# Kernel optimization log

Hardware: AMD Instinct MI355X
Metric: run time of the kernel (lower is better)

The kernel has to match this reference:

```python
import jax, jax.numpy as jnp
import numpy as np

TOP_K = 2


def setup_inputs() -> dict:
    key = jax.random.key(0)
    k_x, k_g, k_w1, k_w2, k_w3 = jax.random.split(key, 5)
    B, S, D, H, E = 2, 512, 1024, 512, 8
    x = jax.random.normal(k_x, (B, S, D), dtype=jnp.float32)
    gate_w = jax.random.normal(k_g, (D, E), dtype=jnp.float32) * (D ** -0.5)
    w1 = jax.random.normal(k_w1, (E, D, H), dtype=jnp.float32) * 0.02  # gate proj
    w2 = jax.random.normal(k_w2, (E, H, D), dtype=jnp.float32) * 0.02  # down proj
    w3 = jax.random.normal(k_w3, (E, D, H), dtype=jnp.float32) * 0.02  # up proj
    return {"x": x, "gate_w": gate_w, "w1": w1, "w2": w2, "w3": w3}


def reference(x, gate_w, w1, w2, w3):
    # Token-choice top-k MoE with grouped SwiGLU experts, no shared expert.
    # Equivalent to torchtune MoE: gather routed tokens, scale by top-k router
    # score, run per-expert FFN, scatter-add back. Since each expert's FFN has
    # no bias (FFN(0) == 0), the dispatch/grouped-GEMM/combine is expressed
    # densely as sum_e FFN_e(scale[:, e] * x), which is mathematically identical.
    B, S, D = x.shape
    E = gate_w.shape[1]
    xf = x.reshape(B * S, D)                      # [T, D]
    T = B * S

    logits = xf @ gate_w                          # [T, E]
    scores = jax.nn.softmax(logits, axis=-1)
    top_scores, top_idx = jax.lax.top_k(scores, TOP_K)  # [T, k]

    # scale[t, e] = router score if expert e selected for token t, else 0
    scale = jnp.zeros((T, E), dtype=x.dtype).at[
        jnp.arange(T)[:, None], top_idx
    ].set(top_scores)

    xs = scale.T[:, :, None] * xf[None, :, :]     # [E, T, D] scaled routed input
    h = jax.nn.silu(jnp.einsum('etd,edh->eth', xs, w1)) \
        * jnp.einsum('etd,edh->eth', xs, w3)      # [E, T, H]
    y = jnp.einsum('eth,ehd->etd', h, w2)         # [E, T, D]
    out = y.sum(axis=0)                           # combine (scatter-add equiv)
    return out.reshape(B, S, D)
```

## Files before the change

### kernel.cpp

```cpp
#include <hip/hip_runtime.h>
#include <hip/hip_bf16.h>
#include <cstddef>

#define T_TOK 1024
#define D_DIM 1024
#define H_DIM 512
#define E_EXP 8
#define P_CAP 2560
#define MAX_MT 72
#define LDA 72

typedef __attribute__((ext_vector_type(4))) float    float4_t;
typedef __attribute__((ext_vector_type(8))) short    short8_t;
typedef __attribute__((ext_vector_type(4))) unsigned uint4_t;

__device__ __forceinline__ short f2bf(float f) {
  union { float f; unsigned u; } v; v.f = f;
  unsigned u = v.u;
  u += 0x7FFFu + ((u >> 16) & 1u);
  return (short)(u >> 16);
}

__device__ __forceinline__ unsigned pkbf(float a, float b) {
  union { __hip_bfloat162 h; unsigned u; } v;
  v.h = __float22bfloat162_rn(make_float2(a, b));
  return v.u;
}

__global__ __launch_bounds__(256) void prep_kernel(
    const float* __restrict__ w1, const float* __restrict__ w3,
    const float* __restrict__ w2, const float* __restrict__ x,
    const float* __restrict__ gw, short* __restrict__ w13t,
    short* __restrict__ w2t, int* __restrict__ idx2,
    float* __restrict__ scale2, float* __restrict__ out) {
  __shared__ float tile[64][69];
  const int z = blockIdx.z;
  const int tid = threadIdx.x;

  if (z < 24) {
    const float* src; short* dst; int N, ldd, row_off;
    if (z < 16) {
      if (blockIdx.y >= 8) return;
      int which = z >> 3, e = z & 7;
      src = (which ? w3 : w1) + (size_t)e * D_DIM * H_DIM;
      dst = w13t + (size_t)e * D_DIM * (2 * H_DIM);
      N = H_DIM; ldd = D_DIM; row_off = which ? H_DIM : 0;
    } else {
      if (blockIdx.x >= 8) return;
      int e = z - 16;
      src = w2 + (size_t)e * H_DIM * D_DIM;
      dst = w2t + (size_t)e * D_DIM * H_DIM;
      N = D_DIM; ldd = H_DIM; row_off = 0;
    }
    const int k0 = blockIdx.x * 64, n0 = blockIdx.y * 64;
    const int kr = tid >> 4, nc = (tid & 15) * 4;
    #pragma unroll
    for (int p = 0; p < 4; ++p) {
      int k = p * 16 + kr;
      float4_t v = *(const float4_t*)(src + (size_t)(k0 + k) * N + n0 + nc);
      tile[k][nc]     = v[0];
      tile[k][nc + 1] = v[1];
      tile[k][nc + 2] = v[2];
      tile[k][nc + 3] = v[3];
    }
    __syncthreads();
    const int r8 = tid >> 3, c8 = tid & 7;
    #pragma unroll
    for (int p = 0; p < 2; ++p) {
      int row = p * 32 + r8;
      uint4_t u;
      #pragma unroll
      for (int jj = 0; jj < 4; ++jj)
        u[jj] = pkbf(tile[c8 * 8 + 2 * jj][row], tile[c8 * 8 + 2 * jj + 1][row]);
      *(uint4_t*)(dst + (size_t)(row_off + n0 + row) * ldd + k0 + c8 * 8) = u;
    }
    return;
  }

  if (z == 25) {
    float4_t z4 = {0.f, 0.f, 0.f, 0.f};
    float4_t* o = (float4_t*)(out + ((size_t)(blockIdx.y * 16 + blockIdx.x)) * 4096);
    #pragma unroll
    for (int i = 0; i < 4; ++i) o[i * 256 + tid] = z4;
    return;
  }

  const int wid  = tid >> 6;
  const int lane = tid & 63;
  const int t = (blockIdx.y * 16 + blockIdx.x) * 4 + wid;
  const float* xr = x + (size_t)t * D_DIM;
  float acc[E_EXP];
  #pragma unroll
  for (int e = 0; e < E_EXP; ++e) acc[e] = 0.f;
  for (int d = lane; d < D_DIM; d += 64) {
    float xv = xr[d];
    float4_t g0 = *(const float4_t*)(gw + d * E_EXP);
    float4_t g1 = *(const float4_t*)(gw + d * E_EXP + 4);
    acc[0] += xv * g0[0]; acc[1] += xv * g0[1];
    acc[2] += xv * g0[2]; acc[3] += xv * g0[3];
    acc[4] += xv * g1[0]; acc[5] += xv * g1[1];
    acc[6] += xv * g1[2]; acc[7] += xv * g1[3];
  }
  #pragma unroll
  for (int off = 32; off >= 1; off >>= 1) {
    #pragma unroll
    for (int e = 0; e < E_EXP; ++e) acc[e] += __shfl_down(acc[e], off, 64);
  }
  if (lane == 0) {
    float m = acc[0];
    #pragma unroll
    for (int e = 1; e < E_EXP; ++e) m = fmaxf(m, acc[e]);
    float p[E_EXP]; float s = 0.f;
    #pragma unroll
    for (int e = 0; e < E_EXP; ++e) { p[e] = __expf(acc[e] - m); s += p[e]; }
    float inv = 1.f / s;
    #pragma unroll
    for (int e = 0; e < E_EXP; ++e) p[e] *= inv;
    int i1 = 0;
    #pragma unroll
    for (int e = 1; e < E_EXP; ++e) if (p[e] > p[i1]) i1 = e;
    int i2 = (i1 == 0) ? 1 : 0;
    #pragma unroll
    for (int e = 0; e < E_EXP; ++e) {
      if (e == i1 || e == i2) continue;
      if (p[e] > p[i2]) i2 = e;
    }
    idx2[2 * t]     = i1;  scale2[2 * t]     = p[i1];
    idx2[2 * t + 1] = i2;  scale2[2 * t + 1] = p[i2];
  }
}

__global__ __launch_bounds__(256) void scan_kernel(
    const int* __restrict__ idx2, const float* __restrict__ scale2,
    int* __restrict__ pair_tok, float* __restrict__ pair_scale,
    int* __restrict__ meta) {
  __shared__ int cnt[E_EXP], base[E_EXP], cur[E_EXP];
  const int tid = threadIdx.x;
  if (tid < E_EXP) { cnt[tid] = 0; cur[tid] = 0; }
  for (int p = tid; p < P_CAP; p += 256) { pair_tok[p] = -1; pair_scale[p] = 0.f; }
  __syncthreads();
  for (int t = tid; t < T_TOK; t += 256) {
    atomicAdd(&cnt[idx2[2 * t]], 1);
    atomicAdd(&cnt[idx2[2 * t + 1]], 1);
  }
  __syncthreads();
  if (tid == 0) {
    int b = 0, g = 0;
    for (int e = 0; e < E_EXP; ++e) {
      base[e] = b;
      int al = (cnt[e] + 31) & ~31;
      for (int j = 0; j < al; j += 32) { meta[1 + g] = e; meta[81 + g] = b + j; ++g; }
      b += al;
    }
    meta[0] = g;
  }
  __syncthreads();
  for (int t = tid; t < T_TOK; t += 256) {
    #pragma unroll
    for (int s = 0; s < 2; ++s) {
      int e = idx2[2 * t + s];
      int p = base[e] + atomicAdd(&cur[e], 1);
      pair_tok[p] = t;
      pair_scale[p] = scale2[2 * t + s];
    }
  }
}

__global__ __launch_bounds__(256, 6) void gemm1_kernel(
    const float* __restrict__ x, const short* __restrict__ w13t,
    const int* __restrict__ pair_tok, const float* __restrict__ pair_scale,
    const int* __restrict__ meta, short* __restrict__ h) {
  __shared__ short As[32 * LDA];
  __shared__ short B1s[32 * LDA];
  __shared__ short B3s[32 * LDA];
  const int mt = blockIdx.y;
  if (mt >= meta[0]) return;
  const int e    = meta[1 + mt];
  const int row0 = meta[81 + mt];
  const int n0   = blockIdx.x * 32;
  const int tid = threadIdx.x, lane = tid & 63, wid = tid >> 6;
  const int wr = wid >> 1, wc = wid & 1;
  const int q = lane >> 4, ln = lane & 15;
  const short* bsrc = w13t + (size_t)e * D_DIM * (2 * H_DIM);

  const int ar = tid >> 3, ak = (tid & 7) * 8;
  const int   tokr = pair_tok[row0 + ar];
  const float sc   = pair_scale[row0 + ar];
  const float* xrow = x + (size_t)(tokr < 0 ? 0 : tokr) * D_DIM + ak;
  const int br = tid >> 3, bu = (tid & 7) * 8;
  const short* b1p = bsrc + (size_t)(n0 + br) * D_DIM + bu;
  const short* b3p = bsrc + (size_t)(H_DIM + n0 + br) * D_DIM + bu;

  float4_t acc1 = {0.f, 0.f, 0.f, 0.f}, acc3 = {0.f, 0.f, 0.f, 0.f};

  for (int k0 = 0; k0 < D_DIM; k0 += 64) {
    float4_t v0 = *(const float4_t*)(xrow + k0);
    float4_t v1 = *(const float4_t*)(xrow + k0 + 4);
    uint4_t vb1 = *(const uint4_t*)(b1p + k0);
    uint4_t vb3 = *(const uint4_t*)(b3p + k0);
    uint4_t u0 = {pkbf(v0[0] * sc, v0[1] * sc), pkbf(v0[2] * sc, v0[3] * sc),
                  pkbf(v1[0] * sc, v1[1] * sc), pkbf(v1[2] * sc, v1[3] * sc)};
    *(uint4_t*)&As[ar * LDA + ak]  = u0;
    *(uint4_t*)&B1s[br * LDA + bu] = vb1;
    *(uint4_t*)&B3s[br * LDA + bu] = vb3;
    __syncthreads();

    short8_t af[2], b1f[2], b3f[2];
    #pragma unroll
    for (int kk = 0; kk < 2; ++kk) {
      af[kk]  = *(const short8_t*)&As[(wr * 16 + ln) * LDA + kk * 32 + q * 8];
      b1f[kk] = *(const short8_t*)&B1s[(wc * 16 + ln) * LDA + kk * 32 + q * 8];
      b3f[kk] = *(const short8_t*)&B3s[(wc * 16 + ln) * LDA + kk * 32 + q * 8];
    }
    #pragma unroll
    for (int kk = 0; kk < 2; ++kk) {
      acc1 = __builtin_amdgcn_mfma_f32_16x16x32_bf16(af[kk], b1f[kk], acc1, 0, 0, 0);
      acc3 = __builtin_amdgcn_mfma_f32_16x16x32_bf16(af[kk], b3f[kk], acc3, 0, 0, 0);
    }
    __syncthreads();
  }

  {
    int r_base = row0 + wr * 16 + q * 4;
    int col = n0 + wc * 16 + ln;
    #pragma unroll
    for (int rr = 0; rr < 4; ++rr) {
      float c1 = acc1[rr];
      float c3 = acc3[rr];
      float sig = 1.f / (1.f + __expf(-c1));
      h[(size_t)(r_base + rr) * H_DIM + col] = f2bf(c1 * sig * c3);
    }
  }
}

__global__ __launch_bounds__(256, 6) void gemm2_kernel(
    const short* __restrict__ h, const short* __restrict__ w2t,
    const int* __restrict__ pair_tok, const int* __restrict__ meta,
    float* __restrict__ out) {
  __shared__ short As[32 * LDA];
  __shared__ short Bs[64 * LDA];
  const int mt = blockIdx.y;
  if (mt >= meta[0]) return;
  const int e    = meta[1 + mt];
  const int row0 = meta[81 + mt];
  const int n0   = blockIdx.x * 64;
  const int tid = threadIdx.x, lane = tid & 63, wid = tid >> 6;
  const int wr = wid >> 1, wc = wid & 1;
  const int q = lane >> 4, ln = lane & 15;
  const short* bsrc = w2t + (size_t)e * D_DIM * H_DIM;

  const int ar = tid >> 3, ak = (tid & 7) * 8;
  const short* arow = h + (size_t)(row0 + ar) * H_DIM + ak;
  const int br = tid >> 2, bk = (tid & 3) * 16;
  const short* brow = bsrc + (size_t)(n0 + br) * H_DIM + bk;

  float4_t acc[2];
  acc[0] = acc[1] = (float4_t){0.f, 0.f, 0.f, 0.f};

  for (int k0 = 0; k0 < H_DIM; k0 += 64) {
    uint4_t va  = *(const uint4_t*)(arow + k0);
    uint4_t vb0 = *(const uint4_t*)(brow + k0);
    uint4_t vb1 = *(const uint4_t*)(brow + k0 + 8);
    *(uint4_t*)&As[ar * LDA + ak]     = va;
    *(uint4_t*)&Bs[br * LDA + bk]     = vb0;
    *(uint4_t*)&Bs[br * LDA + bk + 8] = vb1;
    __syncthreads();

    short8_t af[2], bf[2][2];
    #pragma unroll
    for (int kk = 0; kk < 2; ++kk) {
      af[kk] = *(const short8_t*)&As[(wr * 16 + ln) * LDA + kk * 32 + q * 8];
      #pragma unroll
      for (int j = 0; j < 2; ++j)
        bf[j][kk] = *(const short8_t*)&Bs[(wc * 32 + j * 16 + ln) * LDA + kk * 32 + q * 8];
    }
    #pragma unroll
    for (int j = 0; j < 2; ++j)
      #pragma unroll
      for (int kk = 0; kk < 2; ++kk)
        acc[j] = __builtin_amdgcn_mfma_f32_16x16x32_bf16(af[kk], bf[j][kk], acc[j], 0, 0, 0);
    __syncthreads();
  }

  {
    int r_base = row0 + wr * 16 + q * 4;
    #pragma unroll
    for (int rr = 0; rr < 4; ++rr) {
      int tok = pair_tok[r_base + rr];
      if (tok < 0) continue;
      float* orow = out + (size_t)tok * D_DIM;
      #pragma unroll
      for (int j = 0; j < 2; ++j) {
        int col = n0 + wc * 32 + j * 16 + ln;
        atomicAdd(orow + col, acc[j][rr]);
      }
    }
  }
}

extern "C" void kernel_launch(void* const* d_in, const int* in_sizes, int n_in,
                              void* d_out, int out_size, void* d_ws, size_t ws_size,
                              hipStream_t stream) {
  const float* x  = (const float*)d_in[0];
  const float* gw = (const float*)d_in[1];
  const float* w1 = (const float*)d_in[2];
  const float* w2 = (const float*)d_in[3];
  const float* w3 = (const float*)d_in[4];
  float* out = (float*)d_out;

  char* ws = (char*)d_ws;
  int*   idx2    = (int*)  (ws);
  float* scale2  = (float*)(ws + 8192);
  int*   ptok    = (int*)  (ws + 16384);
  float* pscale  = (float*)(ws + 32768);
  int*   meta    = (int*)  (ws + 49152);
  short* h       = (short*)(ws + (1u << 20));
  short* w13t    = (short*)(ws + (4u << 20));
  short* w2t     = (short*)(ws + (21u << 20));

  prep_kernel<<<dim3(16, 16, 26), dim3(256), 0, stream>>>(
      w1, w3, w2, x, gw, w13t, w2t, idx2, scale2, out);
  scan_kernel<<<dim3(1), dim3(256), 0, stream>>>(idx2, scale2, ptok, pscale, meta);
  gemm1_kernel<<<dim3(H_DIM / 32, MAX_MT), dim3(256), 0, stream>>>(
      x, w13t, ptok, pscale, meta, h);
  gemm2_kernel<<<dim3(D_DIM / 64, MAX_MT), dim3(256), 0, stream>>>(
      h, w2t, ptok, meta, out);
}
```

Before: 146.7 us.

## Double-buffer LDS in both GEMMs and pre-stage scaled bf16 routed activations

```diff
diff --git a/kernel.cpp b/kernel.cpp
--- a/kernel.cpp
+++ b/kernel.cpp
@@ -9,10 +9,13 @@
 #define P_CAP 2560
 #define MAX_MT 72
 #define LDA 72
+#define NK1 16
+#define NK2 8
 
 typedef __attribute__((ext_vector_type(4))) float    float4_t;
 typedef __attribute__((ext_vector_type(8))) short    short8_t;
 typedef __attribute__((ext_vector_type(4))) unsigned uint4_t;
+typedef __attribute__((ext_vector_type(2))) unsigned uint2_t;
 
 __device__ __forceinline__ short f2bf(float f) {
   union { float f; unsigned u; } v; v.f = f;
@@ -166,13 +169,31 @@
   }
 }
 
-__global__ __launch_bounds__(256, 6) void gemm1_kernel(
-    const float* __restrict__ x, const short* __restrict__ w13t,
-    const int* __restrict__ pair_tok, const float* __restrict__ pair_scale,
+__global__ __launch_bounds__(256) void astage_kernel(
+    const float* __restrict__ x, const int* __restrict__ pair_tok,
+    const float* __restrict__ pair_scale, short* __restrict__ Ag) {
+  const int tid = threadIdx.x;
+  const int row = blockIdx.x * 8 + (tid >> 5);
+  const int c0  = (tid & 31) * 4;
+  const int   tok = pair_tok[row];
+  const float sc  = pair_scale[row];
+  const float* xr = x + (size_t)(tok < 0 ? 0 : tok) * D_DIM;
+  short* orow = Ag + (size_t)row * D_DIM;
+  #pragma unroll
+  for (int j = 0; j < 8; ++j) {
+    int c = c0 + j * 128;
+    float4_t v = *(const float4_t*)(xr + c);
+    uint2_t u = { pkbf(v[0] * sc, v[1] * sc), pkbf(v[2] * sc, v[3] * sc) };
+    *(uint2_t*)(orow + c) = u;
+  }
+}
+
+__global__ __launch_bounds__(256, 5) void gemm1_kernel(
+    const short* __restrict__ Ag, const short* __restrict__ w13t,
     const int* __restrict__ meta, short* __restrict__ h) {
-  __shared__ short As[32 * LDA];
-  __shared__ short B1s[32 * LDA];
-  __shared__ short B3s[32 * LDA];
+  __shared__ short As[2][32 * LDA];
+  __shared__ short B1s[2][32 * LDA];
+  __shared__ short B3s[2][32 * LDA];
   const int mt = blockIdx.y;
   if (mt >= meta[0]) return;
   const int e    = meta[1 + mt];
@@ -183,41 +204,60 @@
   const int q = lane >> 4, ln = lane & 15;
   const short* bsrc = w13t + (size_t)e * D_DIM * (2 * H_DIM);
 
-  const int ar = tid >> 3, ak = (tid & 7) * 8;
-  const int   tokr = pair_tok[row0 + ar];
-  const float sc   = pair_scale[row0 + ar];
-  const float* xrow = x + (size_t)(tokr < 0 ? 0 : tokr) * D_DIM + ak;
-  const int br = tid >> 3, bu = (tid & 7) * 8;
-  const short* b1p = bsrc + (size_t)(n0 + br) * D_DIM + bu;
-  const short* b3p = bsrc + (size_t)(H_DIM + n0 + br) * D_DIM + bu;
+  const int sr = tid >> 3, sk = (tid & 7) * 8;
+  const short* ap  = Ag   + (size_t)(row0 + sr) * D_DIM + sk;
+  const short* b1p = bsrc + (size_t)(n0 + sr) * D_DIM + sk;
+  const short* b3p = bsrc + (size_t)(H_DIM + n0 + sr) * D_DIM + sk;
 
   float4_t acc1 = {0.f, 0.f, 0.f, 0.f}, acc3 = {0.f, 0.f, 0.f, 0.f};
 
-  for (int k0 = 0; k0 < D_DIM; k0 += 64) {
-    float4_t v0 = *(const float4_t*)(xrow + k0);
-    float4_t v1 = *(const float4_t*)(xrow + k0 + 4);
-    uint4_t vb1 = *(const uint4_t*)(b1p + k0);
-    uint4_t vb3 = *(const uint4_t*)(b3p + k0);
-    uint4_t u0 = {pkbf(v0[0] * sc, v0[1] * sc), pkbf(v0[2] * sc, v0[3] * sc),
-                  pkbf(v1[0] * sc, v1[1] * sc), pkbf(v1[2] * sc, v1[3] * sc)};
-    *(uint4_t*)&As[ar * LDA + ak]  = u0;
-    *(uint4_t*)&B1s[br * LDA + bu] = vb1;
-    *(uint4_t*)&B3s[br * LDA + bu] = vb3;
+  {
+    uint4_t va = *(const uint4_t*)ap;
+    uint4_t v1 = *(const uint4_t*)b1p;
+    uint4_t v3 = *(const uint4_t*)b3p;
+    *(uint4_t*)&As[0][sr * LDA + sk]  = va;
+    *(uint4_t*)&B1s[0][sr * LDA + sk] = v1;
+    *(uint4_t*)&B3s[0][sr * LDA + sk] = v3;
+  }
+
+  for (int t = 0; t < NK1 - 1; ++t) {
     __syncthreads();
+    const int cur = t & 1, nxt = cur ^ 1;
+    const int ko = (t + 1) * 64;
+    uint4_t wa  = *(const uint4_t*)(ap + ko);
+    uint4_t w1v = *(const uint4_t*)(b1p + ko);
+    uint4_t w3v = *(const uint4_t*)(b3p + ko);
 
     short8_t af[2], b1f[2], b3f[2];
     #pragma unroll
     for (int kk = 0; kk < 2; ++kk) {
-      af[kk]  = *(const short8_t*)&As[(wr * 16 + ln) * LDA + kk * 32 + q * 8];
-      b1f[kk] = *(const short8_t*)&B1s[(wc * 16 + ln) * LDA + kk * 32 + q * 8];
-      b3f[kk] = *(const short8_t*)&B3s[(wc * 16 + ln) * LDA + kk * 32 + q * 8];
+      af[kk]  = *(const short8_t*)&As[cur][(wr * 16 + ln) * LDA + kk * 32 + q * 8];
+      b1f[kk] = *(const short8_t*)&B1s[cur][(wc * 16 + ln) * LDA + kk * 32 + q * 8];
+      b3f[kk] = *(const short8_t*)&B3s[cur][(wc * 16 + ln) * LDA + kk * 32 + q * 8];
     }
     #pragma unroll
     for (int kk = 0; kk < 2; ++kk) {
       acc1 = __builtin_amdgcn_mfma_f32_16x16x32_bf16(af[kk], b1f[kk], acc1, 0, 0, 0);
       acc3 = __builtin_amdgcn_mfma_f32_16x16x32_bf16(af[kk], b3f[kk], acc3, 0, 0, 0);
     }
-    __syncthreads();
+    *(uint4_t*)&As[nxt][sr * LDA + sk]  = wa;
+    *(uint4_t*)&B1s[nxt][sr * LDA + sk] = w1v;
+    *(uint4_t*)&B3s[nxt][sr * LDA + sk] = w3v;
+  }
+  __syncthreads();
+  {
+    short8_t af[2], b1f[2], b3f[2];
+    #pragma unroll
+    for (int kk = 0; kk < 2; ++kk) {
+      af[kk]  = *(const short8_t*)&As[1][(wr * 16 + ln) * LDA + kk * 32 + q * 8];
+      b1f[kk] = *(const short8_t*)&B1s[1][(wc * 16 + ln) * LDA + kk * 32 + q * 8];
+      b3f[kk] = *(const short8_t*)&B3s[1][(wc * 16 + ln) * LDA + kk * 32 + q * 8];
+    }
+    #pragma unroll
+    for (int kk = 0; kk < 2; ++kk) {
+      acc1 = __builtin_amdgcn_mfma_f32_16x16x32_bf16(af[kk], b1f[kk], acc1, 0, 0, 0);
+      acc3 = __builtin_amdgcn_mfma_f32_16x16x32_bf16(af[kk], b3f[kk], acc3, 0, 0, 0);
+    }
   }
 
   {
@@ -233,12 +273,12 @@
   }
 }
 
-__global__ __launch_bounds__(256, 6) void gemm2_kernel(
+__global__ __launch_bounds__(256, 5) void gemm2_kernel(
     const short* __restrict__ h, const short* __restrict__ w2t,
     const int* __restrict__ pair_tok, const int* __restrict__ meta,
     float* __restrict__ out) {
-  __shared__ short As[32 * LDA];
-  __shared__ short Bs[64 * LDA];
+  __shared__ short As[2][32 * LDA];
+  __shared__ short Bs[2][64 * LDA];
   const int mt = blockIdx.y;
   if (mt >= meta[0]) return;
   const int e    = meta[1 + mt];
@@ -257,29 +297,56 @@
   float4_t acc[2];
   acc[0] = acc[1] = (float4_t){0.f, 0.f, 0.f, 0.f};
 
-  for (int k0 = 0; k0 < H_DIM; k0 += 64) {
-    uint4_t va  = *(const uint4_t*)(arow + k0);
-    uint4_t vb0 = *(const uint4_t*)(brow + k0);
-    uint4_t vb1 = *(const uint4_t*)(brow + k0 + 8);
-    *(uint4_t*)&As[ar * LDA + ak]     = va;
-    *(uint4_t*)&Bs[br * LDA + bk]     = vb0;
-    *(uint4_t*)&Bs[br * LDA + bk + 8] = vb1;
+  {
+    uint4_t va  = *(const uint4_t*)arow;
+    uint4_t vb0 = *(const uint4_t*)brow;
+    uint4_t vb1 = *(const uint4_t*)(brow + 8);
+    *(uint4_t*)&As[0][ar * LDA + ak]     = va;
+    *(uint4_t*)&Bs[0][br * LDA + bk]     = vb0;
+    *(uint4_t*)&Bs[0][br * LDA + bk + 8] = vb1;
+  }
+
+  for (int t = 0; t < NK2 - 1; ++t) {
     __syncthreads();
+    const int cur = t & 1, nxt = cur ^ 1;
+    const int ko = (t + 1) * 64;
+    uint4_t wa  = *(const uint4_t*)(arow + ko);
+    uint4_t wb0 = *(const uint4_t*)(brow + ko);
+    uint4_t wb1 = *(const uint4_t*)(brow + ko + 8);
 
     short8_t af[2], bf[2][2];
     #pragma unroll
     for (int kk = 0; kk < 2; ++kk) {
-      af[kk] = *(const short8_t*)&As[(wr * 16 + ln) * LDA + kk * 32 + q * 8];
+      af[kk] = *(const short8_t*)&As[cur][(wr * 16 + ln) * LDA + kk * 32 + q * 8];
       #pragma unroll
       for (int j = 0; j < 2; ++j)
-        bf[j][kk] = *(const short8_t*)&Bs[(wc * 32 + j * 16 + ln) * LDA + kk * 32 + q * 8];
+        bf[j][kk] = *(const short8_t*)&Bs[cur][(wc * 32 + j * 16 + ln) * LDA + kk * 32 + q * 8];
     }
     #pragma unroll
     for (int j = 0; j < 2; ++j)
       #pragma unroll
       for (int kk = 0; kk < 2; ++kk)
         acc[j] = __builtin_amdgcn_mfma_f32_16x16x32_bf16(af[kk], bf[j][kk], acc[j], 0, 0, 0);
-    __syncthreads();
+
+    *(uint4_t*)&As[nxt][ar * LDA + ak]     = wa;
+    *(uint4_t*)&Bs[nxt][br * LDA + bk]     = wb0;
+    *(uint4_t*)&Bs[nxt][br * LDA + bk + 8] = wb1;
+  }
+  __syncthreads();
+  {
+    short8_t af[2], bf[2][2];
+    #pragma unroll
+    for (int kk = 0; kk < 2; ++kk) {
+      af[kk] = *(const short8_t*)&As[1][(wr * 16 + ln) * LDA + kk * 32 + q * 8];
+      #pragma unroll
+      for (int j = 0; j < 2; ++j)
+        bf[j][kk] = *(const short8_t*)&Bs[1][(wc * 32 + j * 16 + ln) * LDA + kk * 32 + q * 8];
+    }
+    #pragma unroll
+    for (int j = 0; j < 2; ++j)
+      #pragma unroll
+      for (int kk = 0; kk < 2; ++kk)
+        acc[j] = __builtin_amdgcn_mfma_f32_16x16x32_bf16(af[kk], bf[j][kk], acc[j], 0, 0, 0);
   }
 
   {
@@ -317,12 +384,14 @@
   short* h       = (short*)(ws + (1u << 20));
   short* w13t    = (short*)(ws + (4u << 20));
   short* w2t     = (short*)(ws + (21u << 20));
+  short* Ag      = (short*)(ws + (30u << 20));
 
   prep_kernel<<<dim3(16, 16, 26), dim3(256), 0, stream>>>(
       w1, w3, w2, x, gw, w13t, w2t, idx2, scale2, out);
   scan_kernel<<<dim3(1), dim3(256), 0, stream>>>(idx2, scale2, ptok, pscale, meta);
+  astage_kernel<<<dim3(P_CAP / 8), dim3(256), 0, stream>>>(x, ptok, pscale, Ag);
   gemm1_kernel<<<dim3(H_DIM / 32, MAX_MT), dim3(256), 0, stream>>>(
-      x, w13t, ptok, pscale, meta, h);
+      Ag, w13t, meta, h);
   gemm2_kernel<<<dim3(D_DIM / 64, MAX_MT), dim3(256), 0, stream>>>(
       h, w2t, ptok, meta, out);
 }
```

After: 147.3 us. Within noise of the previous version (+0.4%).
